# Kernel optimization log

Hardware: AMD Instinct MI355X
Metric: run time of the kernel (lower is better)

## Reference

```python
import jax, jax.numpy as jnp
import numpy as np

B, S, D, H = 2, 2048, 1024, 16
HD = D // H
SCALE = HD ** -0.5


def setup_inputs() -> dict:
    key = jax.random.key(0)
    ks = jax.random.split(key, 11)
    std = D ** -0.5
    inp = {
        'query': jax.random.normal(ks[0], (B, S, D), jnp.float32),
        'key': jax.random.normal(ks[1], (B, S, D), jnp.float32),
        'value': jax.random.normal(ks[2], (B, S, D), jnp.float32),
        'Wq': jax.random.normal(ks[3], (D, D), jnp.float32) * std,
        'bq': jnp.zeros((D,), jnp.float32),
        'Wk': jax.random.normal(ks[4], (D, D), jnp.float32) * std,
        'bk': jnp.zeros((D,), jnp.float32),
        'Wv': jax.random.normal(ks[5], (D, D), jnp.float32) * std,
        'bv': jnp.zeros((D,), jnp.float32),
        'Wo': jax.random.normal(ks[6], (D, D), jnp.float32) * std,
        'bo': jnp.zeros((D,), jnp.float32),
    }
    return inp


def reference(query, key, value, Wq, bq, Wk, bk, Wv, bv, Wo, bo):
    # Linear projections (torch Linear: x @ W.T + b), split into heads -> [B,H,S,HD]
    def proj(x, W, b):
        y = jnp.einsum('bsd,ed->bse', x, W) + b
        return y.reshape(B, S, H, HD).transpose(0, 2, 1, 3)

    Q = proj(query, Wq, bq)
    K = proj(key, Wk, bk)
    V = proj(value, Wv, bv)
    scores = jnp.einsum('bhqd,bhkd->bhqk', Q, K) * SCALE  # [B,H,S,S]
    attn = jax.nn.softmax(scores, axis=-1)
    ctx = jnp.einsum('bhqk,bhkd->bhqd', attn, V)
    ctx = ctx.transpose(0, 2, 1, 3).reshape(B, S, D)
    out = jnp.einsum('bsd,ed->bse', ctx, Wo) + bo
    return out
```

## Files before the change

kernel.cpp:

```cpp
#include <hip/hip_runtime.h>
#include <hip/hip_bf16.h>

#define DEVFN __device__ __forceinline__

typedef __attribute__((ext_vector_type(8))) short bf16x8;
typedef __attribute__((ext_vector_type(4))) float f32x4;
typedef __attribute__((ext_vector_type(16))) float f32x16;

constexpr int Bc = 2, Sc = 2048, Dc = 1024, Hc = 16, HDc = 64;
constexpr float SCALEc = 0.125f;
constexpr float LOG2E  = 1.44269504088896340736f;

DEVFN unsigned short f2bf(float f) {
    union { float f; unsigned int u; } x; x.f = f;
    return (unsigned short)((x.u + 0x7fffu + ((x.u >> 16) & 1u)) >> 16);
}

DEVFN f32x4 mfma16(bf16x8 a, bf16x8 b, f32x4 c) {
    return __builtin_amdgcn_mfma_f32_16x16x32_bf16(a, b, c, 0, 0, 0);
}
DEVFN f32x16 mfma32(bf16x8 a, bf16x8 b, f32x16 c) {
    return __builtin_amdgcn_mfma_f32_32x32x16_bf16(a, b, c, 0, 0, 0);
}

DEVFN void gload16(const void* g, void* l) {
    __builtin_amdgcn_global_load_lds((const __attribute__((address_space(1))) void*)g,
                                     (__attribute__((address_space(3))) void*)l, 16, 0, 0);
}

__global__ __launch_bounds__(256) void cvt_w(
    const float* __restrict__ wq, const float* __restrict__ wk,
    const float* __restrict__ wv, const float* __restrict__ wo,
    unsigned short* __restrict__ wqb, unsigned short* __restrict__ wkb,
    unsigned short* __restrict__ wvb, unsigned short* __restrict__ wob)
{
    const unsigned t = blockIdx.x * 256 + threadIdx.x;
    const unsigned which = t >> 17, local = t & ((1u << 17) - 1);
    const float* s = which == 0 ? wq : which == 1 ? wk : which == 2 ? wv : wo;
    unsigned short* d = which == 0 ? wqb : which == 1 ? wkb : which == 2 ? wvb : wob;
    const size_t off = (size_t)local * 8;
    float4 v0 = *(const float4*)(s + off);
    float4 v1 = *(const float4*)(s + off + 4);
    unsigned short t8[8] = {f2bf(v0.x), f2bf(v0.y), f2bf(v0.z), f2bf(v0.w),
                            f2bf(v1.x), f2bf(v1.y), f2bf(v1.z), f2bf(v1.w)};
    *(uint4*)(d + off) = *(const uint4*)t8;
}

__global__ __launch_bounds__(256, 3) void qkv_gemm(
    const float* __restrict__ Aq, const float* __restrict__ Ak, const float* __restrict__ Av,
    const unsigned short* __restrict__ Wqb, const unsigned short* __restrict__ Wkb,
    const unsigned short* __restrict__ Wvb,
    const float* __restrict__ bqp, const float* __restrict__ bkp, const float* __restrict__ bvp,
    unsigned short* __restrict__ Qo, unsigned short* __restrict__ Ko, unsigned short* __restrict__ Vto)
{
    __shared__ short As[2][4096];
    __shared__ short Bs[2][4096];

    const int lgid = (blockIdx.x & 7) * 96 + (blockIdx.x >> 3);
    const int g = lgid >> 8;
    const int rem = lgid & 255;
    const int tm = rem >> 3, tn = rem & 7;

    const float* A = g == 0 ? Aq : g == 1 ? Ak : Av;
    const unsigned short* Bw = g == 0 ? Wqb : g == 1 ? Wkb : Wvb;
    const float* bias = g == 0 ? bqp : g == 1 ? bkp : bvp;
    const float scale = g == 0 ? SCALEc * LOG2E : 1.0f;

    const int tid = threadIdx.x, lane = tid & 63, w = tid >> 6;
    const int lr = lane & 15, lg = lane >> 4;
    const int wm = (w >> 1) * 64, wn = (w & 1) * 64;

    const int c0 = 2 * w, c1 = 2 * w + 1;
    const int r0 = c0 * 16 + (lane >> 2), r1 = c1 * 16 + (lane >> 2);
    const int s0 = (lane & 3) ^ ((r0 >> 1) & 3), s1 = (lane & 3) ^ ((r1 >> 1) & 3);
    const float* Afp0 = A + (size_t)(tm * 128 + r0) * 1024 + s0 * 8;
    const float* Afp1 = A + (size_t)(tm * 128 + r1) * 1024 + s1 * 8;
    const unsigned short* Bp0 = Bw + (size_t)(tn * 128 + r0) * 1024 + s0 * 8;
    const unsigned short* Bp1 = Bw + (size_t)(tn * 128 + r1) * 1024 + s1 * 8;
    short* AW0[2] = {&As[0][c0 * 512 + lane * 8], &As[1][c0 * 512 + lane * 8]};
    short* AW1[2] = {&As[0][c1 * 512 + lane * 8], &As[1][c1 * 512 + lane * 8]};

    f32x4 acc[4][4] = {};
    const int fread = (lr >> 1) & 3;

    float4 fE[4], fO[4];

    fE[0] = *(const float4*)(Afp0);     fE[1] = *(const float4*)(Afp0 + 4);
    fE[2] = *(const float4*)(Afp1);     fE[3] = *(const float4*)(Afp1 + 4);
    gload16(Bp0, &Bs[0][c0 * 512]);
    gload16(Bp1, &Bs[0][c1 * 512]);
    {
        unsigned int q0, q1, q2, q3;
        asm("v_cvt_pk_bf16_f32 %0,%1,%2" : "=v"(q0) : "v"(fE[0].x), "v"(fE[0].y));
        asm("v_cvt_pk_bf16_f32 %0,%1,%2" : "=v"(q1) : "v"(fE[0].z), "v"(fE[0].w));
        asm("v_cvt_pk_bf16_f32 %0,%1,%2" : "=v"(q2) : "v"(fE[1].x), "v"(fE[1].y));
        asm("v_cvt_pk_bf16_f32 %0,%1,%2" : "=v"(q3) : "v"(fE[1].z), "v"(fE[1].w));
        *(uint4*)AW0[0] = (uint4){q0, q1, q2, q3};
        asm("v_cvt_pk_bf16_f32 %0,%1,%2" : "=v"(q0) : "v"(fE[2].x), "v"(fE[2].y));
        asm("v_cvt_pk_bf16_f32 %0,%1,%2" : "=v"(q1) : "v"(fE[2].z), "v"(fE[2].w));
        asm("v_cvt_pk_bf16_f32 %0,%1,%2" : "=v"(q2) : "v"(fE[3].x), "v"(fE[3].y));
        asm("v_cvt_pk_bf16_f32 %0,%1,%2" : "=v"(q3) : "v"(fE[3].z), "v"(fE[3].w));
        *(uint4*)AW1[0] = (uint4){q0, q1, q2, q3};
    }
    fO[0] = *(const float4*)(Afp0 + 32); fO[1] = *(const float4*)(Afp0 + 36);
    fO[2] = *(const float4*)(Afp1 + 32); fO[3] = *(const float4*)(Afp1 + 36);
    asm volatile("s_waitcnt lgkmcnt(0)" ::: "memory");

#define QKV_STEP(KT, P, FI, FC)                                                  \
    {                                                                            \
        const int k1 = ((KT) < 31) ? ((KT) + 1) * 32 : 992;                      \
        const int k2 = ((KT) < 30) ? ((KT) + 2) * 32 : 992;                      \
        gload16(Bp0 + k1, &Bs[(P) ^ 1][c0 * 512]);                               \
        gload16(Bp1 + k1, &Bs[(P) ^ 1][c1 * 512]);                               \
        FI[0] = *(const float4*)(Afp0 + k2); FI[1] = *(const float4*)(Afp0 + k2 + 4); \
        FI[2] = *(const float4*)(Afp1 + k2); FI[3] = *(const float4*)(Afp1 + k2 + 4); \
        asm volatile("s_waitcnt vmcnt(10)" ::: "memory");                        \
        __builtin_amdgcn_s_barrier();                                            \
        __builtin_amdgcn_sched_barrier(0);                                       \
        const short* Ac  = As[P];                                                \
        const short* Bc2 = Bs[P];                                                \
        bf16x8 af[4], bfv[4];                                                    \
        _Pragma("unroll")                                                        \
        for (int m = 0; m < 4; m++) {                                            \
            const int row = wm + m * 16 + lr;                                    \
            af[m] = *(const bf16x8*)&Ac[row * 32 + (lg ^ fread) * 8];            \
        }                                                                        \
        _Pragma("unroll")                                                        \
        for (int n = 0; n < 4; n++) {                                            \
            const int row = wn + n * 16 + lr;                                    \
            bfv[n] = *(const bf16x8*)&Bc2[row * 32 + (lg ^ fread) * 8];          \
        }                                                                        \
        _Pragma("unroll")                                                        \
        for (int m = 0; m < 4; m++)                                              \
            _Pragma("unroll")                                                    \
            for (int n = 0; n < 4; n++)                                          \
                acc[m][n] = mfma16(af[m], bfv[n], acc[m][n]);                    \
        {                                                                        \
            unsigned int q0, q1, q2, q3;                                         \
            asm("v_cvt_pk_bf16_f32 %0,%1,%2" : "=v"(q0) : "v"(FC[0].x), "v"(FC[0].y)); \
            asm("v_cvt_pk_bf16_f32 %0,%1,%2" : "=v"(q1) : "v"(FC[0].z), "v"(FC[0].w)); \
            asm("v_cvt_pk_bf16_f32 %0,%1,%2" : "=v"(q2) : "v"(FC[1].x), "v"(FC[1].y)); \
            asm("v_cvt_pk_bf16_f32 %0,%1,%2" : "=v"(q3) : "v"(FC[1].z), "v"(FC[1].w)); \
            *(uint4*)AW0[(P) ^ 1] = (uint4){q0, q1, q2, q3};                     \
            asm("v_cvt_pk_bf16_f32 %0,%1,%2" : "=v"(q0) : "v"(FC[2].x), "v"(FC[2].y)); \
            asm("v_cvt_pk_bf16_f32 %0,%1,%2" : "=v"(q1) : "v"(FC[2].z), "v"(FC[2].w)); \
            asm("v_cvt_pk_bf16_f32 %0,%1,%2" : "=v"(q2) : "v"(FC[3].x), "v"(FC[3].y)); \
            asm("v_cvt_pk_bf16_f32 %0,%1,%2" : "=v"(q3) : "v"(FC[3].z), "v"(FC[3].w)); \
            *(uint4*)AW1[(P) ^ 1] = (uint4){q0, q1, q2, q3};                     \
        }                                                                        \
        asm volatile("s_waitcnt lgkmcnt(0)" ::: "memory");                       \
        __builtin_amdgcn_sched_barrier(0);                                       \
        __builtin_amdgcn_s_barrier();                                            \
    }

    for (int kt = 0; kt < 32; kt += 2) {
        QKV_STEP(kt,     0, fE, fO)
        QKV_STEP(kt + 1, 1, fO, fE)
    }
    asm volatile("s_waitcnt vmcnt(0)" ::: "memory");
#undef QKV_STEP

    if (g < 2) {
        unsigned short* Y = g == 0 ? Qo : Ko;
        #pragma unroll
        for (int n = 0; n < 4; n++) {
            const int col = tn * 128 + wn + n * 16 + lr;
            const float bv = bias[col];
            const int hh = col >> 6, hd = col & 63;
            #pragma unroll
            for (int m = 0; m < 4; m++) {
                const int row0 = tm * 128 + wm + m * 16 + lg * 4;
                const int b_ = row0 >> 11, sQ = row0 & 2047;
                #pragma unroll
                for (int r = 0; r < 4; r++) {
                    const float val = (acc[m][n][r] + bv) * scale;
                    Y[(((size_t)(b_ * Hc + hh)) * Sc + (sQ + r)) * HDc + hd] = f2bf(val);
                }
            }
        }
    } else {
        #pragma unroll
        for (int n = 0; n < 4; n++) {
            const int col = tn * 128 + wn + n * 16 + lr;
            const float bv = bias[col];
            const int hh = col >> 6, hd = col & 63;
            #pragma unroll
            for (int m = 0; m < 4; m++) {
                const int row0 = tm * 128 + wm + m * 16 + lg * 4;
                const int b_ = row0 >> 11, sQ = row0 & 2047;
                const int sQp = (sQ & ~12) | ((sQ & 4) << 1) | ((sQ & 8) >> 1);
                unsigned long long pk = 0;
                #pragma unroll
                for (int r = 0; r < 4; r++)
                    pk |= (unsigned long long)f2bf(acc[m][n][r] + bv) << (16 * r);
                *(unsigned long long*)&Vto[(((size_t)(b_ * Hc + hh)) * HDc + hd) * Sc + sQp] = pk;
            }
        }
    }
}

__global__ __launch_bounds__(256) void out_gemm(
    const unsigned short* __restrict__ Ab, const unsigned short* __restrict__ Bw,
    const float* __restrict__ bias, float* __restrict__ Y)
{
    __shared__ short As[2][4096];
    __shared__ short Bs[2][4096];
    const int tid = threadIdx.x, lane = tid & 63, w = tid >> 6;
    const int lr = lane & 15, lg = lane >> 4;
    const int lgid = (blockIdx.x & 7) * 32 + (blockIdx.x >> 3);
    const int tm = lgid >> 3, tn = lgid & 7;
    const int wm = (w >> 1) * 64, wn = (w & 1) * 64;

    const int c0 = 2 * w, c1 = 2 * w + 1;
    const int r0 = c0 * 16 + (lane >> 2), r1 = c1 * 16 + (lane >> 2);
    const int sl0 = ((lane & 3) ^ ((r0 >> 1) & 3)) * 8, sl1 = ((lane & 3) ^ ((r1 >> 1) & 3)) * 8;
    const unsigned short* Ap0 = Ab + (size_t)(tm * 128 + r0) * 1024 + sl0;
    const unsigned short* Ap1 = Ab + (size_t)(tm * 128 + r1) * 1024 + sl1;
    const unsigned short* Bp0 = Bw + (size_t)(tn * 128 + r0) * 1024 + sl0;
    const unsigned short* Bp1 = Bw + (size_t)(tn * 128 + r1) * 1024 + sl1;

    f32x4 acc[4][4] = {};
    const int fread = (lr >> 1) & 3;

    gload16(Ap0, &As[0][c0 * 512]);
    gload16(Ap1, &As[0][c1 * 512]);
    gload16(Bp0, &Bs[0][c0 * 512]);
    gload16(Bp1, &Bs[0][c1 * 512]);

    int cur = 0;
    for (int k0 = 0; k0 < 1024; k0 += 32) {
        const int nk = (k0 + 32 < 1024) ? k0 + 32 : k0;
        gload16(Ap0 + nk, &As[cur ^ 1][c0 * 512]);
        gload16(Ap1 + nk, &As[cur ^ 1][c1 * 512]);
        gload16(Bp0 + nk, &Bs[cur ^ 1][c0 * 512]);
        gload16(Bp1 + nk, &Bs[cur ^ 1][c1 * 512]);
        asm volatile("s_waitcnt vmcnt(4)" ::: "memory");
        __builtin_amdgcn_s_barrier();
        __builtin_amdgcn_sched_barrier(0);

        const short* Ac  = As[cur];
        const short* Bc2 = Bs[cur];
        bf16x8 af[4], bfv[4];
        #pragma unroll
        for (int m = 0; m < 4; m++) {
            const int row = wm + m * 16 + lr;
            af[m] = *(const bf16x8*)&Ac[row * 32 + (lg ^ fread) * 8];
        }
        #pragma unroll
        for (int n = 0; n < 4; n++) {
            const int row = wn + n * 16 + lr;
            bfv[n] = *(const bf16x8*)&Bc2[row * 32 + (lg ^ fread) * 8];
        }
        #pragma unroll
        for (int m = 0; m < 4; m++)
            #pragma unroll
            for (int n = 0; n < 4; n++)
                acc[m][n] = mfma16(af[m], bfv[n], acc[m][n]);

        asm volatile("s_waitcnt lgkmcnt(0)" ::: "memory");
        __builtin_amdgcn_sched_barrier(0);
        __builtin_amdgcn_s_barrier();
        cur ^= 1;
    }
    asm volatile("s_waitcnt vmcnt(0)" ::: "memory");

    #pragma unroll
    for (int n = 0; n < 4; n++) {
        const int col = tn * 128 + wn + n * 16 + lr;
        const float bv = bias[col];
        #pragma unroll
        for (int m = 0; m < 4; m++) {
            const int row0 = tm * 128 + wm + m * 16 + lg * 4;
            #pragma unroll
            for (int r = 0; r < 4; r++)
                Y[(size_t)(row0 + r) * 1024 + col] = acc[m][n][r] + bv;
        }
    }
}

__global__ __launch_bounds__(512, 2) void attn_fwd(
    const unsigned short* __restrict__ Q, const unsigned short* __restrict__ Kg,
    const unsigned short* __restrict__ Vtg, unsigned short* __restrict__ ctx)
{
    __shared__ short Ks[2][4096];
    __shared__ short Vs[2][4096];

    const int tid = threadIdx.x, lane = tid & 63, w = tid >> 6;
    const int l31 = lane & 31, hi = lane >> 5;

    const int blk = blockIdx.x;
    const int idx = blk >> 3;
    const int bh = (blk & 7) * 4 + (idx >> 3);
    const int qt = idx & 7;

    const unsigned short* Qb = Q   + (size_t)bh * Sc * HDc;
    const unsigned short* Kb = Kg  + (size_t)bh * Sc * HDc;
    const unsigned short* Vb = Vtg + (size_t)bh * HDc * Sc;

    const int qbase = qt * 256 + w * 32;
    bf16x8 qf[4];
    {
        const size_t qr = (size_t)(qbase + l31) * HDc + hi * 8;
        #pragma unroll
        for (int kk = 0; kk < 4; kk++)
            qf[kk] = *(const bf16x8*)&Qb[qr + kk * 16];
    }

    const int srow  = w * 8 + (lane >> 3);
    const int sslot = ((lane & 7) ^ (lane >> 3)) * 8;
    const unsigned short* Kst = Kb + (size_t)srow * HDc + sslot;
    const unsigned short* Vst = Vb + (size_t)srow * Sc + sslot;

    const int swk = lane & 7;

    const f32x16 Z = {};
    f32x16 acc0 = {}, acc1 = {}, accl = {};

    union { unsigned int u[4]; bf16x8 v; } ones;
    ones.u[0] = ones.u[1] = ones.u[2] = ones.u[3] = 0x3F803F80u;

    gload16(Kst, &Ks[0][w * 512]);
    gload16(Vst, &Vs[0][w * 512]);

    int cur = 0;
    for (int kt = 0; kt < 32; ++kt) {
        {
            const int nxt = kt < 31 ? kt + 1 : 31;
            gload16(Kst + (size_t)nxt * 4096, &Ks[cur ^ 1][w * 512]);
            gload16(Vst + nxt * 64,           &Vs[cur ^ 1][w * 512]);
        }
        asm volatile("s_waitcnt vmcnt(2)" ::: "memory");
        __builtin_amdgcn_s_barrier();
        __builtin_amdgcn_sched_barrier(0);

        const short* Kc = Ks[cur];
        const short* Vc = Vs[cur];

        f32x16 sf0, sf1;
        __builtin_amdgcn_s_setprio(1);
        {
            const int sl = (hi ^ swk) * 8;
            bf16x8 a0 = *(const bf16x8*)&Kc[l31 * 64 + sl];
            bf16x8 a1 = *(const bf16x8*)&Kc[(32 + l31) * 64 + sl];
            sf0 = mfma32(a0, qf[0], Z);
            sf1 = mfma32(a1, qf[0], Z);
        }
        #pragma unroll
        for (int kk = 1; kk < 4; kk++) {
            const int sl = ((2 * kk + hi) ^ swk) * 8;
            bf16x8 a0 = *(const bf16x8*)&Kc[l31 * 64 + sl];
            bf16x8 a1 = *(const bf16x8*)&Kc[(32 + l31) * 64 + sl];
            sf0 = mfma32(a0, qf[kk], sf0);
            sf1 = mfma32(a1, qf[kk], sf1);
        }
        __builtin_amdgcn_s_setprio(0);

        unsigned int p0[8], p1[8];
        #pragma unroll
        for (int j = 0; j < 8; j++) {
            const float a0 = __builtin_amdgcn_exp2f(sf0[2 * j]);
            const float a1 = __builtin_amdgcn_exp2f(sf0[2 * j + 1]);
            const float b0 = __builtin_amdgcn_exp2f(sf1[2 * j]);
            const float b1 = __builtin_amdgcn_exp2f(sf1[2 * j + 1]);
            asm("v_cvt_pk_bf16_f32 %0, %1, %2" : "=v"(p0[j]) : "v"(a0), "v"(a1));
            asm("v_cvt_pk_bf16_f32 %0, %1, %2" : "=v"(p1[j]) : "v"(b0), "v"(b1));
        }

        __builtin_amdgcn_s_setprio(1);
        #pragma unroll
        for (int m = 0; m < 4; m++) {
            const unsigned int* pw = (m < 2) ? &p0[(m & 1) * 4] : &p1[(m & 1) * 4];
            union { unsigned int u[4]; bf16x8 v; } af;
            af.u[0] = pw[0]; af.u[1] = pw[1]; af.u[2] = pw[2]; af.u[3] = pw[3];
            const int sl = ((2 * m + hi) ^ swk) * 8;
            bf16x8 b0 = *(const bf16x8*)&Vc[l31 * 64 + sl];
            bf16x8 b1 = *(const bf16x8*)&Vc[(32 + l31) * 64 + sl];
            acc0 = mfma32(af.v, b0, acc0);
            acc1 = mfma32(af.v, b1, acc1);
            accl = mfma32(af.v, ones.v, accl);
        }
        __builtin_amdgcn_s_setprio(0);

        asm volatile("s_waitcnt lgkmcnt(0)" ::: "memory");
        __builtin_amdgcn_sched_barrier(0);
        __builtin_amdgcn_s_barrier();
        cur ^= 1;
    }
    asm volatile("s_waitcnt vmcnt(0)" ::: "memory");

    const int b_ = bh >> 4, hh = bh & 15;
    #pragma unroll
    for (int r = 0; r < 16; r++) {
        const int qr = (r & 3) + 8 * (r >> 2) + 4 * hi;
        const float lv = __builtin_amdgcn_rcpf(accl[r]);
        const int sq = qbase + qr;
        unsigned short* co = &ctx[((size_t)(b_ * Sc + sq)) * Dc + (size_t)hh * HDc + l31];
        co[0]  = f2bf(acc0[r] * lv);
        co[32] = f2bf(acc1[r] * lv);
    }
}

extern "C" void kernel_launch(void* const* d_in, const int* in_sizes, int n_in,
                              void* d_out, int out_size, void* d_ws, size_t ws_size,
                              hipStream_t stream)
{
    const float* query = (const float*)d_in[0];
    const float* key   = (const float*)d_in[1];
    const float* value = (const float*)d_in[2];
    const float* Wq = (const float*)d_in[3];
    const float* bq = (const float*)d_in[4];
    const float* Wk = (const float*)d_in[5];
    const float* bk = (const float*)d_in[6];
    const float* Wv = (const float*)d_in[7];
    const float* bv = (const float*)d_in[8];
    const float* Wo = (const float*)d_in[9];
    const float* bo = (const float*)d_in[10];

    constexpr size_t W = 1048576, AE = 4194304;
    unsigned short* wqb = (unsigned short*)d_ws;
    unsigned short* wkb = wqb + W;
    unsigned short* wvb = wkb + W;
    unsigned short* wob = wvb + W;
    unsigned short* Qh  = wob + W;
    unsigned short* Kh  = Qh + AE;
    unsigned short* Vth = Kh + AE;
    unsigned short* cx  = Vth + AE;

    cvt_w<<<2048, 256, 0, stream>>>(Wq, Wk, Wv, Wo, wqb, wkb, wvb, wob);
    qkv_gemm<<<768, 256, 0, stream>>>(query, key, value, wqb, wkb, wvb,
                                      bq, bk, bv, Qh, Kh, Vth);
    attn_fwd<<<256, 512, 0, stream>>>(Qh, Kh, Vth, cx);
    out_gemm<<<256, 256, 0, stream>>>(cx, wob, bo, (float*)d_out);
}
```

Baseline: 115.6 us.

## Triple/quad-buffer LDS stages to drop trailing barrier per iteration

The two GEMM kernels move from double to triple LDS buffering, and the attention kernel moves from double to quad buffering with a prefetch distance of two. This lets each loop iteration drop its second workgroup barrier, since the buffer being written is never the one still being read. The attention kernel now has two tiles of loads in flight. The cost is more LDS per block, which may lower occupancy, and the correctness of the rotation depends on the single remaining barrier protecting reuse of each buffer.

```diff
diff --git a/kernel.cpp b/kernel.cpp
--- a/kernel.cpp
+++ b/kernel.cpp
@@ -53,8 +53,8 @@
     const float* __restrict__ bqp, const float* __restrict__ bkp, const float* __restrict__ bvp,
     unsigned short* __restrict__ Qo, unsigned short* __restrict__ Ko, unsigned short* __restrict__ Vto)
 {
-    __shared__ short As[2][4096];
-    __shared__ short Bs[2][4096];
+    __shared__ short As[3 * 4096];
+    __shared__ short Bs[3 * 4096];
 
     const int lgid = (blockIdx.x & 7) * 96 + (blockIdx.x >> 3);
     const int g = lgid >> 8;
@@ -77,48 +77,51 @@
     const float* Afp1 = A + (size_t)(tm * 128 + r1) * 1024 + s1 * 8;
     const unsigned short* Bp0 = Bw + (size_t)(tn * 128 + r0) * 1024 + s0 * 8;
     const unsigned short* Bp1 = Bw + (size_t)(tn * 128 + r1) * 1024 + s1 * 8;
-    short* AW0[2] = {&As[0][c0 * 512 + lane * 8], &As[1][c0 * 512 + lane * 8]};
-    short* AW1[2] = {&As[0][c1 * 512 + lane * 8], &As[1][c1 * 512 + lane * 8]};
+    const int aw0 = c0 * 512 + lane * 8;
+    const int aw1 = c1 * 512 + lane * 8;
 
     f32x4 acc[4][4] = {};
     const int fread = (lr >> 1) & 3;
 
     float4 fE[4], fO[4];
 
+#define CVT_A(R, WOFS)                                                           \
+    {                                                                            \
+        unsigned int q0, q1, q2, q3;                                             \
+        asm("v_cvt_pk_bf16_f32 %0,%1,%2" : "=v"(q0) : "v"(R[0].x), "v"(R[0].y)); \
+        asm("v_cvt_pk_bf16_f32 %0,%1,%2" : "=v"(q1) : "v"(R[0].z), "v"(R[0].w)); \
+        asm("v_cvt_pk_bf16_f32 %0,%1,%2" : "=v"(q2) : "v"(R[1].x), "v"(R[1].y)); \
+        asm("v_cvt_pk_bf16_f32 %0,%1,%2" : "=v"(q3) : "v"(R[1].z), "v"(R[1].w)); \
+        *(uint4*)&As[(WOFS) + aw0] = (uint4){q0, q1, q2, q3};                    \
+        asm("v_cvt_pk_bf16_f32 %0,%1,%2" : "=v"(q0) : "v"(R[2].x), "v"(R[2].y)); \
+        asm("v_cvt_pk_bf16_f32 %0,%1,%2" : "=v"(q1) : "v"(R[2].z), "v"(R[2].w)); \
+        asm("v_cvt_pk_bf16_f32 %0,%1,%2" : "=v"(q2) : "v"(R[3].x), "v"(R[3].y)); \
+        asm("v_cvt_pk_bf16_f32 %0,%1,%2" : "=v"(q3) : "v"(R[3].z), "v"(R[3].w)); \
+        *(uint4*)&As[(WOFS) + aw1] = (uint4){q0, q1, q2, q3};                    \
+    }
+
+    gload16(Bp0, &Bs[c0 * 512]);
+    gload16(Bp1, &Bs[c1 * 512]);
     fE[0] = *(const float4*)(Afp0);     fE[1] = *(const float4*)(Afp0 + 4);
     fE[2] = *(const float4*)(Afp1);     fE[3] = *(const float4*)(Afp1 + 4);
-    gload16(Bp0, &Bs[0][c0 * 512]);
-    gload16(Bp1, &Bs[0][c1 * 512]);
-    {
-        unsigned int q0, q1, q2, q3;
-        asm("v_cvt_pk_bf16_f32 %0,%1,%2" : "=v"(q0) : "v"(fE[0].x), "v"(fE[0].y));
-        asm("v_cvt_pk_bf16_f32 %0,%1,%2" : "=v"(q1) : "v"(fE[0].z), "v"(fE[0].w));
-        asm("v_cvt_pk_bf16_f32 %0,%1,%2" : "=v"(q2) : "v"(fE[1].x), "v"(fE[1].y));
-        asm("v_cvt_pk_bf16_f32 %0,%1,%2" : "=v"(q3) : "v"(fE[1].z), "v"(fE[1].w));
-        *(uint4*)AW0[0] = (uint4){q0, q1, q2, q3};
-        asm("v_cvt_pk_bf16_f32 %0,%1,%2" : "=v"(q0) : "v"(fE[2].x), "v"(fE[2].y));
-        asm("v_cvt_pk_bf16_f32 %0,%1,%2" : "=v"(q1) : "v"(fE[2].z), "v"(fE[2].w));
-        asm("v_cvt_pk_bf16_f32 %0,%1,%2" : "=v"(q2) : "v"(fE[3].x), "v"(fE[3].y));
-        asm("v_cvt_pk_bf16_f32 %0,%1,%2" : "=v"(q3) : "v"(fE[3].z), "v"(fE[3].w));
-        *(uint4*)AW1[0] = (uint4){q0, q1, q2, q3};
-    }
+    CVT_A(fE, 0)
     fO[0] = *(const float4*)(Afp0 + 32); fO[1] = *(const float4*)(Afp0 + 36);
     fO[2] = *(const float4*)(Afp1 + 32); fO[3] = *(const float4*)(Afp1 + 36);
     asm volatile("s_waitcnt lgkmcnt(0)" ::: "memory");
 
-#define QKV_STEP(KT, P, FI, FC)                                                  \
+#define QKV_STEP(KT, RB, WOFS, FI, FC)                                           \
     {                                                                            \
         const int k1 = ((KT) < 31) ? ((KT) + 1) * 32 : 992;                      \
         const int k2 = ((KT) < 30) ? ((KT) + 2) * 32 : 992;                      \
-        gload16(Bp0 + k1, &Bs[(P) ^ 1][c0 * 512]);                               \
-        gload16(Bp1 + k1, &Bs[(P) ^ 1][c1 * 512]);                               \
+        gload16(Bp0 + k1, &Bs[(WOFS) + c0 * 512]);                               \
+        gload16(Bp1 + k1, &Bs[(WOFS) + c1 * 512]);                               \
         FI[0] = *(const float4*)(Afp0 + k2); FI[1] = *(const float4*)(Afp0 + k2 + 4); \
         FI[2] = *(const float4*)(Afp1 + k2); FI[3] = *(const float4*)(Afp1 + k2 + 4); \
         asm volatile("s_waitcnt vmcnt(10)" ::: "memory");                        \
         __builtin_amdgcn_s_barrier();                                            \
         __builtin_amdgcn_sched_barrier(0);                                       \
-        const short* Ac  = As[P];                                                \
-        const short* Bc2 = Bs[P];                                                \
+        const short* Ac  = &As[RB];                                              \
+        const short* Bc2 = &Bs[RB];                                              \
         bf16x8 af[4], bfv[4];                                                    \
         _Pragma("unroll")                                                        \
         for (int m = 0; m < 4; m++) {                                            \
@@ -135,30 +138,22 @@
             _Pragma("unroll")                                                    \
             for (int n = 0; n < 4; n++)                                          \
                 acc[m][n] = mfma16(af[m], bfv[n], acc[m][n]);                    \
-        {                                                                        \
-            unsigned int q0, q1, q2, q3;                                         \
-            asm("v_cvt_pk_bf16_f32 %0,%1,%2" : "=v"(q0) : "v"(FC[0].x), "v"(FC[0].y)); \
-            asm("v_cvt_pk_bf16_f32 %0,%1,%2" : "=v"(q1) : "v"(FC[0].z), "v"(FC[0].w)); \
-            asm("v_cvt_pk_bf16_f32 %0,%1,%2" : "=v"(q2) : "v"(FC[1].x), "v"(FC[1].y)); \
-            asm("v_cvt_pk_bf16_f32 %0,%1,%2" : "=v"(q3) : "v"(FC[1].z), "v"(FC[1].w)); \
-            *(uint4*)AW0[(P) ^ 1] = (uint4){q0, q1, q2, q3};                     \
-            asm("v_cvt_pk_bf16_f32 %0,%1,%2" : "=v"(q0) : "v"(FC[2].x), "v"(FC[2].y)); \
-            asm("v_cvt_pk_bf16_f32 %0,%1,%2" : "=v"(q1) : "v"(FC[2].z), "v"(FC[2].w)); \
-            asm("v_cvt_pk_bf16_f32 %0,%1,%2" : "=v"(q2) : "v"(FC[3].x), "v"(FC[3].y)); \
-            asm("v_cvt_pk_bf16_f32 %0,%1,%2" : "=v"(q3) : "v"(FC[3].z), "v"(FC[3].w)); \
-            *(uint4*)AW1[(P) ^ 1] = (uint4){q0, q1, q2, q3};                     \
-        }                                                                        \
+        CVT_A(FC, WOFS)                                                          \
         asm volatile("s_waitcnt lgkmcnt(0)" ::: "memory");                       \
         __builtin_amdgcn_sched_barrier(0);                                       \
-        __builtin_amdgcn_s_barrier();                                            \
-    }
-
+    }
+
+    int rb = 0;
     for (int kt = 0; kt < 32; kt += 2) {
-        QKV_STEP(kt,     0, fE, fO)
-        QKV_STEP(kt + 1, 1, fO, fE)
+        const int wb0 = rb == 8192 ? 0 : rb + 4096;
+        QKV_STEP(kt, rb, wb0, fE, fO)
+        const int wb1 = wb0 == 8192 ? 0 : wb0 + 4096;
+        QKV_STEP(kt + 1, wb0, wb1, fO, fE)
+        rb = wb1;
     }
     asm volatile("s_waitcnt vmcnt(0)" ::: "memory");
 #undef QKV_STEP
+#undef CVT_A
 
     if (g < 2) {
         unsigned short* Y = g == 0 ? Qo : Ko;
@@ -203,8 +198,8 @@
     const unsigned short* __restrict__ Ab, const unsigned short* __restrict__ Bw,
     const float* __restrict__ bias, float* __restrict__ Y)
 {
-    __shared__ short As[2][4096];
-    __shared__ short Bs[2][4096];
+    __shared__ short As[3 * 4096];
+    __shared__ short Bs[3 * 4096];
     const int tid = threadIdx.x, lane = tid & 63, w = tid >> 6;
     const int lr = lane & 15, lg = lane >> 4;
     const int lgid = (blockIdx.x & 7) * 32 + (blockIdx.x >> 3);
@@ -222,24 +217,25 @@
     f32x4 acc[4][4] = {};
     const int fread = (lr >> 1) & 3;
 
-    gload16(Ap0, &As[0][c0 * 512]);
-    gload16(Ap1, &As[0][c1 * 512]);
-    gload16(Bp0, &Bs[0][c0 * 512]);
-    gload16(Bp1, &Bs[0][c1 * 512]);
-
-    int cur = 0;
+    gload16(Ap0,      &As[c0 * 512]);
+    gload16(Ap1,      &As[c1 * 512]);
+    gload16(Bp0,      &Bs[c0 * 512]);
+    gload16(Bp1,      &Bs[c1 * 512]);
+
+    int rb = 0;
     for (int k0 = 0; k0 < 1024; k0 += 32) {
+        const int wb = rb == 8192 ? 0 : rb + 4096;
         const int nk = (k0 + 32 < 1024) ? k0 + 32 : k0;
-        gload16(Ap0 + nk, &As[cur ^ 1][c0 * 512]);
-        gload16(Ap1 + nk, &As[cur ^ 1][c1 * 512]);
-        gload16(Bp0 + nk, &Bs[cur ^ 1][c0 * 512]);
-        gload16(Bp1 + nk, &Bs[cur ^ 1][c1 * 512]);
+        gload16(Ap0 + nk, &As[wb + c0 * 512]);
+        gload16(Ap1 + nk, &As[wb + c1 * 512]);
+        gload16(Bp0 + nk, &Bs[wb + c0 * 512]);
+        gload16(Bp1 + nk, &Bs[wb + c1 * 512]);
         asm volatile("s_waitcnt vmcnt(4)" ::: "memory");
         __builtin_amdgcn_s_barrier();
         __builtin_amdgcn_sched_barrier(0);
 
-        const short* Ac  = As[cur];
-        const short* Bc2 = Bs[cur];
+        const short* Ac  = &As[rb];
+        const short* Bc2 = &Bs[rb];
         bf16x8 af[4], bfv[4];
         #pragma unroll
         for (int m = 0; m < 4; m++) {
@@ -256,11 +252,7 @@
             #pragma unroll
             for (int n = 0; n < 4; n++)
                 acc[m][n] = mfma16(af[m], bfv[n], acc[m][n]);
-
-        asm volatile("s_waitcnt lgkmcnt(0)" ::: "memory");
-        __builtin_amdgcn_sched_barrier(0);
-        __builtin_amdgcn_s_barrier();
-        cur ^= 1;
+        rb = wb;
     }
     asm volatile("s_waitcnt vmcnt(0)" ::: "memory");
 
@@ -282,8 +274,8 @@
     const unsigned short* __restrict__ Q, const unsigned short* __restrict__ Kg,
     const unsigned short* __restrict__ Vtg, unsigned short* __restrict__ ctx)
 {
-    __shared__ short Ks[2][4096];
-    __shared__ short Vs[2][4096];
+    __shared__ short Ks[4][4096];
+    __shared__ short Vs[4][4096];
 
     const int tid = threadIdx.x, lane = tid & 63, w = tid >> 6;
     const int l31 = lane & 31, hi = lane >> 5;
@@ -319,22 +311,24 @@
     union { unsigned int u[4]; bf16x8 v; } ones;
     ones.u[0] = ones.u[1] = ones.u[2] = ones.u[3] = 0x3F803F80u;
 
-    gload16(Kst, &Ks[0][w * 512]);
-    gload16(Vst, &Vs[0][w * 512]);
-
-    int cur = 0;
+    gload16(Kst,        &Ks[0][w * 512]);
+    gload16(Vst,        &Vs[0][w * 512]);
+    gload16(Kst + 4096, &Ks[1][w * 512]);
+    gload16(Vst + 64,   &Vs[1][w * 512]);
+
     for (int kt = 0; kt < 32; ++kt) {
         {
-            const int nxt = kt < 31 ? kt + 1 : 31;
-            gload16(Kst + (size_t)nxt * 4096, &Ks[cur ^ 1][w * 512]);
-            gload16(Vst + nxt * 64,           &Vs[cur ^ 1][w * 512]);
-        }
-        asm volatile("s_waitcnt vmcnt(2)" ::: "memory");
+            const int nxt = kt < 30 ? kt + 2 : 31;
+            const int wb = (kt + 2) & 3;
+            gload16(Kst + (size_t)nxt * 4096, &Ks[wb][w * 512]);
+            gload16(Vst + nxt * 64,           &Vs[wb][w * 512]);
+        }
+        asm volatile("s_waitcnt vmcnt(4)" ::: "memory");
         __builtin_amdgcn_s_barrier();
         __builtin_amdgcn_sched_barrier(0);
 
-        const short* Kc = Ks[cur];
-        const short* Vc = Vs[cur];
+        const short* Kc = Ks[kt & 3];
+        const short* Vc = Vs[kt & 3];
 
         f32x16 sf0, sf1;
         __builtin_amdgcn_s_setprio(1);
@@ -380,11 +374,6 @@
             accl = mfma32(af.v, ones.v, accl);
         }
         __builtin_amdgcn_s_setprio(0);
-
-        asm volatile("s_waitcnt lgkmcnt(0)" ::: "memory");
-        __builtin_amdgcn_sched_barrier(0);
-        __builtin_amdgcn_s_barrier();
-        cur ^= 1;
     }
     asm volatile("s_waitcnt vmcnt(0)" ::: "memory");
 
```

Result: faster. 107.4 us (-7.2%).
